# Optimization experiments

Measured on AMD Instinct MI355X. Metric: run time of the kernel, lower is better.

The kernel has to match this reference:

```python
import jax, jax.numpy as jnp
import numpy as np

N_NODES = 100000
N_EDGES = 1000000
D_FEAT = 64


def setup_inputs() -> dict:
    key = jax.random.key(0)
    k1, k2, k3 = jax.random.split(key, 3)
    features = jax.random.normal(k1, (N_NODES, D_FEAT), dtype=jnp.float32)
    src = jax.random.randint(k2, (N_EDGES,), 0, N_NODES, dtype=jnp.int64)
    dst = jax.random.randint(k3, (N_EDGES,), 0, N_NODES, dtype=jnp.int64)
    return {"features": features, "src": src, "dst": dst}


def reference(features, src, dst):
    # DGL update_all(copy_u('h','m'), sum('m','h')):
    # out[v] = sum_{(u,v) in E} features[u]
    msgs = features[src]  # [E, D] gather of source node features
    h = jax.ops.segment_sum(msgs, dst, num_segments=N_NODES)  # [N, D] scatter-add
    return h
```

## Files before the change

kernel.cpp:

```cpp
#include <hip/hip_runtime.h>


#define N_NODES   100000
#define N_EDGES   1000000
#define D_FEAT    64
#define NPB       128
#define NPB_SHIFT 7
#define NB        782
#define EPB       2048
#define CH        2048

typedef unsigned int uint;
typedef unsigned short ushort;

__device__ inline ushort f2bf(float f) {
    uint u = __float_as_uint(f);
    uint lsb = (u >> 16) & 1u;
    u += 0x7fffu + lsb;
    return (ushort)(u >> 16);
}

__global__ __launch_bounds__(512) void conv_hist_kernel(const float* __restrict__ feat,
                                                        ushort* __restrict__ bfeat,
                                                        const int* __restrict__ dst,
                                                        int* __restrict__ cnt_table,
                                                        int n4, int n_edges, int pblocks) {
    __shared__ int cnt[NB];
    int t = threadIdx.x;

    if ((int)blockIdx.x >= pblocks) {
        int i = ((int)blockIdx.x - pblocks) * 512 + t;
        if (i < n4) {
            float4 v = ((const float4*)feat)[i];
            ushort4 o;
            o.x = f2bf(v.x); o.y = f2bf(v.y); o.z = f2bf(v.z); o.w = f2bf(v.w);
            ((ushort4*)bfeat)[i] = o;
        }
        return;
    }

    for (int i = t; i < NB; i += 512) cnt[i] = 0;
    __syncthreads();
    int idx = blockIdx.x * EPB + t * 4;
    if (idx < n_edges) {
        int4 d = *reinterpret_cast<const int4*>(dst + idx);
        atomicAdd(&cnt[d.x >> NPB_SHIFT], 1);
        atomicAdd(&cnt[d.y >> NPB_SHIFT], 1);
        atomicAdd(&cnt[d.z >> NPB_SHIFT], 1);
        atomicAdd(&cnt[d.w >> NPB_SHIFT], 1);
    }
    __syncthreads();
    for (int b = t; b < NB; b += 512) cnt_table[blockIdx.x * NB + b] = cnt[b];
}

__global__ __launch_bounds__(512) void scan_a_kernel(int* __restrict__ cnt_table,
                                                     int* __restrict__ btot, int pb_rows) {
    int t = threadIdx.x;
    int bucket = blockIdx.x * 8 + (t >> 6);
    int lane = t & 63;
    if (bucket >= NB) return;
    int run = 0;
#pragma unroll
    for (int c = 0; c < 8; ++c) {
        int r = c * 64 + lane;
        int orig = (r < pb_rows) ? cnt_table[r * NB + bucket] : 0;
        int v = orig;
#pragma unroll
        for (int d = 1; d < 64; d <<= 1) {
            int u = __shfl_up(v, d);
            if (lane >= d) v += u;
        }
        if (r < pb_rows) cnt_table[r * NB + bucket] = v - orig + run;
        run += __shfl(v, 63);
    }
    if (lane == 0) btot[bucket] = run;
}

__global__ __launch_bounds__(1024) void scan_b_kernel(const int* __restrict__ btot,
                                                      int* __restrict__ bases, int n_edges) {
    __shared__ int lds[1024];
    int t = threadIdx.x;
    int v = (t < NB) ? btot[t] : 0;
    lds[t] = v;
    __syncthreads();
    for (int off = 1; off < 1024; off <<= 1) {
        int u = (t >= off) ? lds[t - off] : 0;
        __syncthreads();
        lds[t] += u;
        __syncthreads();
    }
    if (t < NB) bases[t] = lds[t] - v;
    if (t == 0) bases[NB] = n_edges;
}

__global__ __launch_bounds__(512) void partition_kernel(const int* __restrict__ src,
                                                        const int* __restrict__ dst,
                                                        const int* __restrict__ bases,
                                                        const int* __restrict__ cnt_table,
                                                        int* __restrict__ pairs, int n) {
    __shared__ int cur[NB];
    int t = threadIdx.x;
    for (int b = t; b < NB; b += 512)
        cur[b] = bases[b] + cnt_table[blockIdx.x * NB + b];
    __syncthreads();

    int idx = blockIdx.x * EPB + t * 4;
    if (idx < n) {
        int4 s = *reinterpret_cast<const int4*>(src + idx);
        int4 d = *reinterpret_cast<const int4*>(dst + idx);
        int b, p;
        b = d.x >> NPB_SHIFT; p = atomicAdd(&cur[b], 1); pairs[p] = (s.x << NPB_SHIFT) | (d.x & (NPB - 1));
        b = d.y >> NPB_SHIFT; p = atomicAdd(&cur[b], 1); pairs[p] = (s.y << NPB_SHIFT) | (d.y & (NPB - 1));
        b = d.z >> NPB_SHIFT; p = atomicAdd(&cur[b], 1); pairs[p] = (s.z << NPB_SHIFT) | (d.z & (NPB - 1));
        b = d.w >> NPB_SHIFT; p = atomicAdd(&cur[b], 1); pairs[p] = (s.w << NPB_SHIFT) | (d.w & (NPB - 1));
    }
}

__device__ inline float4 bf4_to_f4(uint2 v) {
    float4 r;
    r.x = __uint_as_float(v.x << 16);
    r.y = __uint_as_float(v.x & 0xffff0000u);
    r.z = __uint_as_float(v.y << 16);
    r.w = __uint_as_float(v.y & 0xffff0000u);
    return r;
}

__global__ __launch_bounds__(256) void gather16_kernel(const ushort* __restrict__ bfeat,
                                                       const int* __restrict__ bases,
                                                       const int* __restrict__ pairs,
                                                       float* __restrict__ out,
                                                       int n_nodes) {
    __shared__ int pbuf[CH];
    __shared__ int sorted[CH];
    __shared__ int deg[32];
    __shared__ int sc[32];
    __shared__ int start[33];
    __shared__ int cur[32];

    int bb = blockIdx.x >> 2;
    int q  = blockIdx.x & 3;
    int t = threadIdx.x;
    int grp = t >> 4;
    int l16 = t & 15;
    int lo = bases[bb], hi = bases[bb + 1];
    int node0 = bb * NPB + q * 32;

    bool first = true;
    for (int c = lo; c < hi || first; c += CH) {
        int n = hi - c;
        if (n > CH) n = CH;
        if (n < 0) n = 0;

        if (t < 32) deg[t] = 0;
        __syncthreads();
        for (int i = t; i < n; i += 256) {
            int p = pairs[c + i];
            pbuf[i] = p;
            int r = p & (NPB - 1);
            if ((r >> 5) == q) atomicAdd(&deg[r & 31], 1);
        }
        __syncthreads();
        if (t < 32) sc[t] = deg[t];
        __syncthreads();
        for (int off = 1; off < 32; off <<= 1) {
            int u = (t < 32 && t >= off) ? sc[t - off] : 0;
            __syncthreads();
            if (t < 32) sc[t] += u;
            __syncthreads();
        }
        if (t < 32) { start[t + 1] = sc[t]; cur[t] = sc[t] - deg[t]; }
        if (t == 0) start[0] = 0;
        __syncthreads();
        for (int i = t; i < n; i += 256) {
            int p = pbuf[i];
            int r = p & (NPB - 1);
            if ((r >> 5) == q) {
                int pos = atomicAdd(&cur[r & 31], 1);
                sorted[pos] = p >> NPB_SHIFT;
            }
        }
        __syncthreads();

        for (int r = grp; r < 32; r += 16) {
            int s0 = start[r], e0 = start[r + 1];
            float4 a0 = {0.f, 0.f, 0.f, 0.f}, a1 = a0, a2 = a0, a3 = a0;
            int i = s0;
            for (; i + 4 <= e0; i += 4) {
                int n0 = sorted[i], n1 = sorted[i + 1];
                int n2 = sorted[i + 2], n3 = sorted[i + 3];
                uint2 w0 = *reinterpret_cast<const uint2*>(bfeat + (size_t)n0 * D_FEAT + l16 * 4);
                uint2 w1 = *reinterpret_cast<const uint2*>(bfeat + (size_t)n1 * D_FEAT + l16 * 4);
                uint2 w2 = *reinterpret_cast<const uint2*>(bfeat + (size_t)n2 * D_FEAT + l16 * 4);
                uint2 w3 = *reinterpret_cast<const uint2*>(bfeat + (size_t)n3 * D_FEAT + l16 * 4);
                float4 v0 = bf4_to_f4(w0), v1 = bf4_to_f4(w1);
                float4 v2 = bf4_to_f4(w2), v3 = bf4_to_f4(w3);
                a0.x += v0.x; a0.y += v0.y; a0.z += v0.z; a0.w += v0.w;
                a1.x += v1.x; a1.y += v1.y; a1.z += v1.z; a1.w += v1.w;
                a2.x += v2.x; a2.y += v2.y; a2.z += v2.z; a2.w += v2.w;
                a3.x += v3.x; a3.y += v3.y; a3.z += v3.z; a3.w += v3.w;
            }
            for (; i < e0; ++i) {
                uint2 w = *reinterpret_cast<const uint2*>(bfeat + (size_t)sorted[i] * D_FEAT + l16 * 4);
                float4 v = bf4_to_f4(w);
                a0.x += v.x; a0.y += v.y; a0.z += v.z; a0.w += v.w;
            }
            float4 acc;
            acc.x = (a0.x + a1.x) + (a2.x + a3.x);
            acc.y = (a0.y + a1.y) + (a2.y + a3.y);
            acc.z = (a0.z + a1.z) + (a2.z + a3.z);
            acc.w = (a0.w + a1.w) + (a2.w + a3.w);

            int node = node0 + r;
            if (node < n_nodes) {
                float* o = out + (size_t)node * D_FEAT + l16 * 4;
                if (first) {
                    *reinterpret_cast<float4*>(o) = acc;
                } else {
                    atomicAdd(o + 0, acc.x); atomicAdd(o + 1, acc.y);
                    atomicAdd(o + 2, acc.z); atomicAdd(o + 3, acc.w);
                }
            }
        }
        first = false;
        __syncthreads();
    }
}

__global__ __launch_bounds__(256) void gather32_kernel(const float* __restrict__ feat,
                                                       const int* __restrict__ bases,
                                                       const int* __restrict__ pairs,
                                                       float* __restrict__ out,
                                                       int n_nodes) {
    __shared__ int pbuf[CH];
    __shared__ int sorted[CH];
    __shared__ int deg[32];
    __shared__ int sc[32];
    __shared__ int start[33];
    __shared__ int cur[32];

    int bb = blockIdx.x >> 2;
    int q  = blockIdx.x & 3;
    int t = threadIdx.x;
    int grp = t >> 4, l16 = t & 15;
    int lo = bases[bb], hi = bases[bb + 1];
    int node0 = bb * NPB + q * 32;

    bool first = true;
    for (int c = lo; c < hi || first; c += CH) {
        int n = hi - c;
        if (n > CH) n = CH;
        if (n < 0) n = 0;

        if (t < 32) deg[t] = 0;
        __syncthreads();
        for (int i = t; i < n; i += 256) {
            int p = pairs[c + i];
            pbuf[i] = p;
            int r = p & (NPB - 1);
            if ((r >> 5) == q) atomicAdd(&deg[r & 31], 1);
        }
        __syncthreads();
        if (t < 32) sc[t] = deg[t];
        __syncthreads();
        for (int off = 1; off < 32; off <<= 1) {
            int u = (t < 32 && t >= off) ? sc[t - off] : 0;
            __syncthreads();
            if (t < 32) sc[t] += u;
            __syncthreads();
        }
        if (t < 32) { start[t + 1] = sc[t]; cur[t] = sc[t] - deg[t]; }
        if (t == 0) start[0] = 0;
        __syncthreads();
        for (int i = t; i < n; i += 256) {
            int p = pbuf[i];
            int r = p & (NPB - 1);
            if ((r >> 5) == q) {
                int pos = atomicAdd(&cur[r & 31], 1);
                sorted[pos] = p >> NPB_SHIFT;
            }
        }
        __syncthreads();

        for (int r = grp; r < 32; r += 16) {
            int s0 = start[r], e0 = start[r + 1];
            float4 a0 = {0.f, 0.f, 0.f, 0.f};
            for (int i = s0; i < e0; ++i) {
                const float4 v = *reinterpret_cast<const float4*>(feat + (size_t)sorted[i] * D_FEAT + l16 * 4);
                a0.x += v.x; a0.y += v.y; a0.z += v.z; a0.w += v.w;
            }
            int node = node0 + r;
            if (node < n_nodes) {
                float* o = out + (size_t)node * D_FEAT + l16 * 4;
                if (first) *reinterpret_cast<float4*>(o) = a0;
                else {
                    atomicAdd(o + 0, a0.x); atomicAdd(o + 1, a0.y);
                    atomicAdd(o + 2, a0.z); atomicAdd(o + 3, a0.w);
                }
            }
        }
        first = false;
        __syncthreads();
    }
}

extern "C" void kernel_launch(void* const* d_in, const int* in_sizes, int n_in,
                              void* d_out, int out_size, void* d_ws, size_t ws_size,
                              hipStream_t stream) {
    const float* feat = (const float*)d_in[0];
    const int*   src  = (const int*)d_in[1];
    const int*   dst  = (const int*)d_in[2];
    float*       out  = (float*)d_out;

    const int n_edges = in_sizes[1];
    const int pblocks = (n_edges + EPB - 1) / EPB;
    const int n4 = N_NODES * D_FEAT / 4;
    const int cblocks = (n4 + 511) / 512;
    const int sablocks = (NB + 7) / 8;

    int* cnt_table = (int*)d_ws;
    int* btot      = cnt_table + (size_t)pblocks * NB;
    int* bases     = btot + NB;
    int* pairs     = bases + NB + 1;
    size_t int_cnt = (size_t)pblocks * NB + NB + (NB + 1) + (size_t)n_edges;
    size_t bf_off  = (int_cnt * 4 + 7) & ~(size_t)7;
    ushort* bfeat  = (ushort*)((char*)d_ws + bf_off);
    size_t need = bf_off + (size_t)N_NODES * D_FEAT * 2;

    if (ws_size >= need) {
        conv_hist_kernel<<<pblocks + cblocks, 512, 0, stream>>>(feat, bfeat, dst, cnt_table,
                                                                n4, n_edges, pblocks);
        scan_a_kernel<<<sablocks, 512, 0, stream>>>(cnt_table, btot, pblocks);
        scan_b_kernel<<<1, 1024, 0, stream>>>(btot, bases, n_edges);
        partition_kernel<<<pblocks, 512, 0, stream>>>(src, dst, bases, cnt_table, pairs, n_edges);
        gather16_kernel<<<NB * 4, 256, 0, stream>>>(bfeat, bases, pairs, out, N_NODES);
    } else {
        conv_hist_kernel<<<pblocks, 512, 0, stream>>>(feat, nullptr, dst, cnt_table,
                                                      n4, n_edges, pblocks);
        scan_a_kernel<<<sablocks, 512, 0, stream>>>(cnt_table, btot, pblocks);
        scan_b_kernel<<<1, 1024, 0, stream>>>(btot, bases, n_edges);
        partition_kernel<<<pblocks, 512, 0, stream>>>(src, dst, bases, cnt_table, pairs, n_edges);
        gather32_kernel<<<NB * 4, 256, 0, stream>>>(feat, bases, pairs, out, N_NODES);
    }
}
```

Measured before the change: 73.00 us.

## Merge two scan passes via last-block ticket and move bf16 conversion into partition

```diff
diff --git a/kernel.cpp b/kernel.cpp
--- a/kernel.cpp
+++ b/kernel.cpp
@@ -20,12 +20,87 @@
     return (ushort)(u >> 16);
 }
 
-__global__ __launch_bounds__(512) void conv_hist_kernel(const float* __restrict__ feat,
+__global__ __launch_bounds__(512) void hist_kernel(const int* __restrict__ dst,
+                                                   int* __restrict__ cnt_table,
+                                                   int* __restrict__ ticket, int n) {
+    __shared__ int cnt[NB];
+    int t = threadIdx.x;
+    if (blockIdx.x == 0 && t == 0)
+        __hip_atomic_store(ticket, 0, __ATOMIC_RELAXED, __HIP_MEMORY_SCOPE_AGENT);
+    for (int i = t; i < NB; i += 512) cnt[i] = 0;
+    __syncthreads();
+    int idx = blockIdx.x * EPB + t * 4;
+    if (idx < n) {
+        int4 d = *reinterpret_cast<const int4*>(dst + idx);
+        atomicAdd(&cnt[d.x >> NPB_SHIFT], 1);
+        atomicAdd(&cnt[d.y >> NPB_SHIFT], 1);
+        atomicAdd(&cnt[d.z >> NPB_SHIFT], 1);
+        atomicAdd(&cnt[d.w >> NPB_SHIFT], 1);
+    }
+    __syncthreads();
+    for (int b = t; b < NB; b += 512) cnt_table[blockIdx.x * NB + b] = cnt[b];
+}
+
+__global__ __launch_bounds__(1024) void scan_kernel(int* __restrict__ cnt_table,
+                                                    int* __restrict__ btot,
+                                                    int* __restrict__ bases,
+                                                    int* __restrict__ ticket,
+                                                    int n_edges, int pb_rows, int nblocks) {
+    __shared__ int lds[1024];
+    __shared__ int isLast;
+    int t = threadIdx.x;
+    int wave = t >> 6, lane = t & 63;
+    int bucket = blockIdx.x * 16 + wave;
+
+    if (bucket < NB) {
+        int run = 0;
+#pragma unroll
+        for (int c = 0; c < 8; ++c) {
+            int r = c * 64 + lane;
+            int orig = (r < pb_rows) ? cnt_table[r * NB + bucket] : 0;
+            int v = orig;
+#pragma unroll
+            for (int d = 1; d < 64; d <<= 1) {
+                int u = __shfl_up(v, d);
+                if (lane >= d) v += u;
+            }
+            if (r < pb_rows) cnt_table[r * NB + bucket] = v - orig + run;
+            run += __shfl(v, 63);
+        }
+        if (lane == 0)
+            __hip_atomic_store(&btot[bucket], run, __ATOMIC_RELAXED,
+                               __HIP_MEMORY_SCOPE_AGENT);
+    }
+
+    __threadfence();
+    __syncthreads();
+    if (t == 0) isLast = (atomicAdd(ticket, 1) == nblocks - 1);
+    __syncthreads();
+    if (!isLast) return;
+
+    int v = (t < NB) ? __hip_atomic_load(&btot[t], __ATOMIC_RELAXED,
+                                         __HIP_MEMORY_SCOPE_AGENT) : 0;
+    lds[t] = v;
+    __syncthreads();
+    for (int off = 1; off < 1024; off <<= 1) {
+        int u = (t >= off) ? lds[t - off] : 0;
+        __syncthreads();
+        lds[t] += u;
+        __syncthreads();
+    }
+    if (t < NB) bases[t] = lds[t] - v;
+    if (t == 0) bases[NB] = n_edges;
+}
+
+__global__ __launch_bounds__(512) void part_conv_kernel(const int* __restrict__ src,
+                                                        const int* __restrict__ dst,
+                                                        const int* __restrict__ bases,
+                                                        const int* __restrict__ cnt_table,
+                                                        int* __restrict__ pairs,
+                                                        const float* __restrict__ feat,
                                                         ushort* __restrict__ bfeat,
-                                                        const int* __restrict__ dst,
-                                                        int* __restrict__ cnt_table,
-                                                        int n4, int n_edges, int pblocks) {
-    __shared__ int cnt[NB];
+                                                        int n_edges, int n4, int pblocks) {
+    __shared__ int cur[NB];
     int t = threadIdx.x;
 
     if ((int)blockIdx.x >= pblocks) {
@@ -39,73 +114,12 @@
         return;
     }
 
-    for (int i = t; i < NB; i += 512) cnt[i] = 0;
-    __syncthreads();
+    for (int b = t; b < NB; b += 512)
+        cur[b] = bases[b] + cnt_table[blockIdx.x * NB + b];
+    __syncthreads();
+
     int idx = blockIdx.x * EPB + t * 4;
     if (idx < n_edges) {
-        int4 d = *reinterpret_cast<const int4*>(dst + idx);
-        atomicAdd(&cnt[d.x >> NPB_SHIFT], 1);
-        atomicAdd(&cnt[d.y >> NPB_SHIFT], 1);
-        atomicAdd(&cnt[d.z >> NPB_SHIFT], 1);
-        atomicAdd(&cnt[d.w >> NPB_SHIFT], 1);
-    }
-    __syncthreads();
-    for (int b = t; b < NB; b += 512) cnt_table[blockIdx.x * NB + b] = cnt[b];
-}
-
-__global__ __launch_bounds__(512) void scan_a_kernel(int* __restrict__ cnt_table,
-                                                     int* __restrict__ btot, int pb_rows) {
-    int t = threadIdx.x;
-    int bucket = blockIdx.x * 8 + (t >> 6);
-    int lane = t & 63;
-    if (bucket >= NB) return;
-    int run = 0;
-#pragma unroll
-    for (int c = 0; c < 8; ++c) {
-        int r = c * 64 + lane;
-        int orig = (r < pb_rows) ? cnt_table[r * NB + bucket] : 0;
-        int v = orig;
-#pragma unroll
-        for (int d = 1; d < 64; d <<= 1) {
-            int u = __shfl_up(v, d);
-            if (lane >= d) v += u;
-        }
-        if (r < pb_rows) cnt_table[r * NB + bucket] = v - orig + run;
-        run += __shfl(v, 63);
-    }
-    if (lane == 0) btot[bucket] = run;
-}
-
-__global__ __launch_bounds__(1024) void scan_b_kernel(const int* __restrict__ btot,
-                                                      int* __restrict__ bases, int n_edges) {
-    __shared__ int lds[1024];
-    int t = threadIdx.x;
-    int v = (t < NB) ? btot[t] : 0;
-    lds[t] = v;
-    __syncthreads();
-    for (int off = 1; off < 1024; off <<= 1) {
-        int u = (t >= off) ? lds[t - off] : 0;
-        __syncthreads();
-        lds[t] += u;
-        __syncthreads();
-    }
-    if (t < NB) bases[t] = lds[t] - v;
-    if (t == 0) bases[NB] = n_edges;
-}
-
-__global__ __launch_bounds__(512) void partition_kernel(const int* __restrict__ src,
-                                                        const int* __restrict__ dst,
-                                                        const int* __restrict__ bases,
-                                                        const int* __restrict__ cnt_table,
-                                                        int* __restrict__ pairs, int n) {
-    __shared__ int cur[NB];
-    int t = threadIdx.x;
-    for (int b = t; b < NB; b += 512)
-        cur[b] = bases[b] + cnt_table[blockIdx.x * NB + b];
-    __syncthreads();
-
-    int idx = blockIdx.x * EPB + t * 4;
-    if (idx < n) {
         int4 s = *reinterpret_cast<const int4*>(src + idx);
         int4 d = *reinterpret_cast<const int4*>(dst + idx);
         int b, p;
@@ -315,30 +329,30 @@
     const int pblocks = (n_edges + EPB - 1) / EPB;
     const int n4 = N_NODES * D_FEAT / 4;
     const int cblocks = (n4 + 511) / 512;
-    const int sablocks = (NB + 7) / 8;
+    const int sblocks = (NB + 15) / 16;
 
     int* cnt_table = (int*)d_ws;
     int* btot      = cnt_table + (size_t)pblocks * NB;
     int* bases     = btot + NB;
-    int* pairs     = bases + NB + 1;
-    size_t int_cnt = (size_t)pblocks * NB + NB + (NB + 1) + (size_t)n_edges;
+    int* ticket    = bases + NB + 1;
+    int* pairs     = ticket + 1;
+    size_t int_cnt = (size_t)pblocks * NB + NB + (NB + 1) + 1 + (size_t)n_edges;
     size_t bf_off  = (int_cnt * 4 + 7) & ~(size_t)7;
     ushort* bfeat  = (ushort*)((char*)d_ws + bf_off);
     size_t need = bf_off + (size_t)N_NODES * D_FEAT * 2;
 
+    hist_kernel<<<pblocks, 512, 0, stream>>>(dst, cnt_table, ticket, n_edges);
+    scan_kernel<<<sblocks, 1024, 0, stream>>>(cnt_table, btot, bases, ticket,
+                                              n_edges, pblocks, sblocks);
     if (ws_size >= need) {
-        conv_hist_kernel<<<pblocks + cblocks, 512, 0, stream>>>(feat, bfeat, dst, cnt_table,
-                                                                n4, n_edges, pblocks);
-        scan_a_kernel<<<sablocks, 512, 0, stream>>>(cnt_table, btot, pblocks);
-        scan_b_kernel<<<1, 1024, 0, stream>>>(btot, bases, n_edges);
-        partition_kernel<<<pblocks, 512, 0, stream>>>(src, dst, bases, cnt_table, pairs, n_edges);
+        part_conv_kernel<<<pblocks + cblocks, 512, 0, stream>>>(src, dst, bases, cnt_table,
+                                                                pairs, feat, bfeat,
+                                                                n_edges, n4, pblocks);
         gather16_kernel<<<NB * 4, 256, 0, stream>>>(bfeat, bases, pairs, out, N_NODES);
     } else {
-        conv_hist_kernel<<<pblocks, 512, 0, stream>>>(feat, nullptr, dst, cnt_table,
-                                                      n4, n_edges, pblocks);
-        scan_a_kernel<<<sablocks, 512, 0, stream>>>(cnt_table, btot, pblocks);
-        scan_b_kernel<<<1, 1024, 0, stream>>>(btot, bases, n_edges);
-        partition_kernel<<<pblocks, 512, 0, stream>>>(src, dst, bases, cnt_table, pairs, n_edges);
+        part_conv_kernel<<<pblocks, 512, 0, stream>>>(src, dst, bases, cnt_table,
+                                                      pairs, feat, nullptr,
+                                                      n_edges, n4, pblocks);
         gather32_kernel<<<NB * 4, 256, 0, stream>>>(feat, bases, pairs, out, N_NODES);
     }
 }
```

New measurement: 105.1 us. +44.0%, slower.
